# Performance work log

Measured on AMD Instinct MI355X. Metric: run time of the kernel, lower is better.

## Reference

```python
import jax, jax.numpy as jnp
import numpy as np

N_NODES = 50000
N_EDGES = 800000
IN_NODE = 64
IN_EDGE = 32
HIDDEN = 128
NUM_LAYERS = 3
OUT_DIM = 8
NUM_GRAPHS = 128


def setup_inputs() -> dict:
    key = jax.random.key(0)
    ks = jax.random.split(key, 20)
    inp = {
        "x": jax.random.normal(ks[0], (N_NODES, IN_NODE), dtype=jnp.float32),
        "edge_index": jax.random.randint(ks[1], (2, N_EDGES), 0, N_NODES, dtype=jnp.int32),
        "edge_attr": jax.random.normal(ks[2], (N_EDGES, IN_EDGE), dtype=jnp.float32),
        "batch": jnp.sort(jax.random.randint(ks[3], (N_NODES,), 0, NUM_GRAPHS, dtype=jnp.int32)),
    }
    # MLP params per GINEConv layer: Linear(d_in, H) -> ReLU -> Linear(H, H)
    d_ins = [IN_NODE + IN_EDGE] + [HIDDEN + IN_EDGE] * (NUM_LAYERS - 1)
    for i, d_in in enumerate(d_ins):
        inp[f"w{i}_1"] = jax.random.normal(ks[4 + 3 * i], (d_in, HIDDEN), dtype=jnp.float32) * (1.0 / np.sqrt(d_in))
        inp[f"b{i}_1"] = jnp.zeros((HIDDEN,), dtype=jnp.float32)
        inp[f"w{i}_2"] = jax.random.normal(ks[5 + 3 * i], (HIDDEN, HIDDEN), dtype=jnp.float32) * (1.0 / np.sqrt(HIDDEN))
        inp[f"b{i}_2"] = jnp.zeros((HIDDEN,), dtype=jnp.float32)
    inp["lin_w"] = jax.random.normal(ks[15], (HIDDEN, OUT_DIM), dtype=jnp.float32) * (1.0 / np.sqrt(HIDDEN))
    inp["lin_b"] = jnp.zeros((OUT_DIM,), dtype=jnp.float32)
    return inp


def _gine_conv(x, src, dst, edge_attr, w1, b1, w2, b2):
    # gather source node feats, concat with edge feats, 2-layer MLP, scatter-add to dst
    m = jnp.concatenate([x[src], edge_attr], axis=-1)        # [E, d_in]
    h = jax.nn.relu(m @ w1 + b1) @ w2 + b2                   # [E, H]
    return jax.ops.segment_sum(h, dst, num_segments=N_NODES)  # [N, H]


def reference(x, edge_index, edge_attr, batch,
              w0_1, b0_1, w0_2, b0_2,
              w1_1, b1_1, w1_2, b1_2,
              w2_1, b2_1, w2_2, b2_2,
              lin_w, lin_b):
    src, dst = edge_index[0], edge_index[1]
    layers = [(w0_1, b0_1, w0_2, b0_2), (w1_1, b1_1, w1_2, b1_2), (w2_1, b2_1, w2_2, b2_2)]
    h = x
    for (w1, b1, w2, b2) in layers:
        h = jax.nn.relu(_gine_conv(h, src, dst, edge_attr, w1, b1, w2, b2))
    # global mean pool over graphs
    sums = jax.ops.segment_sum(h, batch, num_segments=NUM_GRAPHS)          # [G, H]
    cnts = jax.ops.segment_sum(jnp.ones((N_NODES,), h.dtype), batch, num_segments=NUM_GRAPHS)
    pooled = sums / jnp.maximum(cnts, 1.0)[:, None]
    return pooled @ lin_w + lin_b
```

## Files before the change

kernel.cpp:

```cpp
#include <hip/hip_runtime.h>
#include <hip/hip_bf16.h>
#include <stdint.h>

typedef __attribute__((ext_vector_type(8))) __bf16 bf16x8;
typedef __attribute__((ext_vector_type(4))) __bf16 bf16x4;
typedef __attribute__((ext_vector_type(4))) float f32x4;

static constexpr int NN = 50000;
static constexpr int NE = 800000;
static constexpr int FX = 64;
static constexpr int FE = 32;
static constexpr int H  = 128;
static constexpr int NG = 128;
static constexpr int OD = 8;

__global__ void cvt_f32_bf16(const float* __restrict__ in, __bf16* __restrict__ out, int n) {
  int idx = (blockIdx.x * blockDim.x + threadIdx.x) * 4;
  if (idx + 3 < n) {
    float4 v = *reinterpret_cast<const float4*>(in + idx);
    bf16x4 o;
    o[0] = (__bf16)v.x; o[1] = (__bf16)v.y; o[2] = (__bf16)v.z; o[3] = (__bf16)v.w;
    *reinterpret_cast<bf16x4*>(out + idx) = o;
  } else {
    for (; idx < n; ++idx) out[idx] = (__bf16)in[idx];
  }
}

__global__ void cvt_w_t(const float* __restrict__ w, __bf16* __restrict__ wt, int K) {
  int i = blockIdx.x * blockDim.x + threadIdx.x;
  if (i >= K * 128) return;
  int n = i / K, k = i % K;
  wt[i] = (__bf16)w[k * 128 + n];
}

__global__ void hist_build(const int* __restrict__ dst, int* __restrict__ hist) {
  int e = blockIdx.x * blockDim.x + threadIdx.x;
  if (e < NE) atomicAdd(&hist[dst[e]], 1);
}

__global__ void scan1(const int* __restrict__ hist, int* __restrict__ excl, int* __restrict__ btot) {
  __shared__ int tmp[256];
  int t = threadIdx.x;
  int i = blockIdx.x * 256 + t;
  int v = (i < NN) ? hist[i] : 0;
  tmp[t] = v;
  __syncthreads();
  for (int off = 1; off < 256; off <<= 1) {
    int add = (t >= off) ? tmp[t - off] : 0;
    __syncthreads();
    tmp[t] += add;
    __syncthreads();
  }
  if (i < NN) excl[i] = tmp[t] - v;
  if (t == 255) btot[blockIdx.x] = tmp[255];
}

__global__ void scan2(int* __restrict__ btot, int nb) {
  __shared__ int tmp[256];
  int t = threadIdx.x;
  int v = (t < nb) ? btot[t] : 0;
  tmp[t] = v;
  __syncthreads();
  for (int off = 1; off < 256; off <<= 1) {
    int add = (t >= off) ? tmp[t - off] : 0;
    __syncthreads();
    tmp[t] += add;
    __syncthreads();
  }
  if (t < nb) btot[t] = tmp[t] - v;
}

__global__ void scan3(const int* __restrict__ excl, const int* __restrict__ btot,
                      int* __restrict__ cursor) {
  int i = blockIdx.x * 256 + threadIdx.x;
  if (i < NN) cursor[i] = excl[i] + btot[blockIdx.x];
}

__global__ void scatter_perm(const int* __restrict__ src, const int* __restrict__ dst,
                             int* __restrict__ cursor,
                             int* __restrict__ srcp, int* __restrict__ dstp,
                             int* __restrict__ eperm) {
  int e = blockIdx.x * blockDim.x + threadIdx.x;
  if (e >= NE) return;
  int d = dst[e];
  int p = atomicAdd(&cursor[d], 1);
  srcp[p] = src[e];
  dstp[p] = d;
  eperm[p] = e;
}

__global__ void sort_ea(const float* __restrict__ ea, const int* __restrict__ eperm,
                        __bf16* __restrict__ eabs) {
  int i = blockIdx.x * blockDim.x + threadIdx.x;
  if (i >= NE * 4) return;
  int p = i >> 2, c = i & 3;
  int e = eperm[p];
  float4 v0 = *reinterpret_cast<const float4*>(ea + (size_t)e * FE + c * 8);
  float4 v1 = *reinterpret_cast<const float4*>(ea + (size_t)e * FE + c * 8 + 4);
  bf16x8 o;
  o[0] = (__bf16)v0.x; o[1] = (__bf16)v0.y; o[2] = (__bf16)v0.z; o[3] = (__bf16)v0.w;
  o[4] = (__bf16)v1.x; o[5] = (__bf16)v1.y; o[6] = (__bf16)v1.z; o[7] = (__bf16)v1.w;
  *reinterpret_cast<bf16x8*>(eabs + (size_t)p * FE + c * 8) = o;
}

template<int F, int DIN>
__global__ __launch_bounds__(512) void node_gemm2(
    const __bf16* __restrict__ Ain,
    const __bf16* __restrict__ wt,
    __bf16* __restrict__ Y)
{
  constexpr int APAD = F + 8;
  constexpr int KS   = F / 32;
  constexpr int CH   = F / 8;
  constexpr int AB   = 128 * APAD * 2;
  constexpr int OB   = 128 * 136 * 2;
  constexpr int SB   = (AB > OB) ? AB : OB;
  __shared__ __align__(16) char smem[SB];
  auto As  = reinterpret_cast<__bf16 (*)[APAD]>(smem);
  auto Ost = reinterpret_cast<__bf16 (*)[136]>(smem);

  const int tid   = threadIdx.x;
  const int lane  = tid & 63;
  const int w     = tid >> 6;
  const int m0    = blockIdx.x * 128;
  const int colq  = lane & 15;
  const int krow  = (lane >> 4) * 8;
  const int rbase = (lane >> 4) * 4;
  const int col   = w * 16 + colq;

  bf16x8 bf[KS];
#pragma unroll
  for (int ks = 0; ks < KS; ++ks)
    bf[ks] = *reinterpret_cast<const bf16x8*>(wt + (size_t)col * DIN + ks * 32 + krow);

  for (int i = tid; i < 128 * CH; i += 512) {
    int row = i / CH, c = i % CH;
    int g = m0 + row; if (g >= NN) g = NN - 1;
    *reinterpret_cast<bf16x8*>(&As[row][c * 8]) =
        *reinterpret_cast<const bf16x8*>(Ain + (size_t)g * F + c * 8);
  }
  __syncthreads();

  f32x4 acc[8];
#pragma unroll
  for (int mt = 0; mt < 8; ++mt) acc[mt] = (f32x4){0.f, 0.f, 0.f, 0.f};
#pragma unroll
  for (int ks = 0; ks < KS; ++ks)
#pragma unroll
    for (int mt = 0; mt < 8; ++mt) {
      bf16x8 a = *reinterpret_cast<const bf16x8*>(&As[mt * 16 + colq][ks * 32 + krow]);
      acc[mt] = __builtin_amdgcn_mfma_f32_16x16x32_bf16(a, bf[ks], acc[mt], 0, 0, 0);
    }
  __syncthreads();

#pragma unroll
  for (int mt = 0; mt < 8; ++mt)
#pragma unroll
    for (int r = 0; r < 4; ++r)
      Ost[mt * 16 + rbase + r][col] = (__bf16)acc[mt][r];
  __syncthreads();

  for (int i = tid; i < 128 * 16; i += 512) {
    int row = i >> 4, c = i & 15;
    int g = m0 + row;
    if (g < NN)
      *reinterpret_cast<bf16x8*>(Y + (size_t)g * H + c * 8) =
          *reinterpret_cast<const bf16x8*>(&Ost[row][c * 8]);
  }
}

template<bool WRITE_Y>
__global__ __launch_bounds__(512) void node_wy(
    const float* __restrict__ aggHin,
    const int* __restrict__ deg,
    const __bf16* __restrict__ w2t,
    const float* __restrict__ b2,
    const __bf16* __restrict__ w1t,
    __bf16* __restrict__ Y,
    float* __restrict__ hpre)
{
  __shared__ __bf16 Ast[128][136];
  __shared__ __bf16 Hst[WRITE_Y ? 128 : 1][136];
  __shared__ int deg_s[128];

  const int tid   = threadIdx.x;
  const int lane  = tid & 63;
  const int w     = tid >> 6;
  const int m0    = blockIdx.x * 128;
  const int colq  = lane & 15;
  const int krow  = (lane >> 4) * 8;
  const int rbase = (lane >> 4) * 4;
  const int col   = w * 16 + colq;

  for (int i = tid; i < 128 * 16; i += 512) {
    int row = i >> 4, cb = (i & 15) * 8;
    int g = m0 + row; if (g >= NN) g = NN - 1;
    const float* s = aggHin + (size_t)g * H + cb;
    float4 v0 = *reinterpret_cast<const float4*>(s);
    float4 v1 = *reinterpret_cast<const float4*>(s + 4);
    bf16x8 o;
    o[0] = (__bf16)v0.x; o[1] = (__bf16)v0.y; o[2] = (__bf16)v0.z; o[3] = (__bf16)v0.w;
    o[4] = (__bf16)v1.x; o[5] = (__bf16)v1.y; o[6] = (__bf16)v1.z; o[7] = (__bf16)v1.w;
    *reinterpret_cast<bf16x8*>(&Ast[row][cb]) = o;
  }
  if (tid < 128) {
    int g = m0 + tid;
    deg_s[tid] = (g < NN) ? deg[g] : 0;
  }
  __syncthreads();

  bf16x8 w2f[4];
#pragma unroll
  for (int ks = 0; ks < 4; ++ks)
    w2f[ks] = *reinterpret_cast<const bf16x8*>(w2t + (size_t)col * H + ks * 32 + krow);
  const float b2s = b2[col];

  f32x4 acc[8];
#pragma unroll
  for (int mt = 0; mt < 8; ++mt) acc[mt] = (f32x4){0.f, 0.f, 0.f, 0.f};
#pragma unroll
  for (int ks = 0; ks < 4; ++ks)
#pragma unroll
    for (int mt = 0; mt < 8; ++mt) {
      bf16x8 a = *reinterpret_cast<const bf16x8*>(&Ast[mt * 16 + colq][ks * 32 + krow]);
      acc[mt] = __builtin_amdgcn_mfma_f32_16x16x32_bf16(a, w2f[ks], acc[mt], 0, 0, 0);
    }

  if (WRITE_Y) {
#pragma unroll
    for (int mt = 0; mt < 8; ++mt)
#pragma unroll
      for (int r = 0; r < 4; ++r) {
        int row = mt * 16 + rbase + r;
        float v = acc[mt][r] + (float)deg_s[row] * b2s;
        Hst[row][col] = (__bf16)fmaxf(v, 0.f);
      }
    __syncthreads();

    bf16x8 w1f[4];
#pragma unroll
    for (int ks = 0; ks < 4; ++ks)
      w1f[ks] = *reinterpret_cast<const bf16x8*>(w1t + (size_t)col * 160 + ks * 32 + krow);

    f32x4 acc2[8];
#pragma unroll
    for (int mt = 0; mt < 8; ++mt) acc2[mt] = (f32x4){0.f, 0.f, 0.f, 0.f};
#pragma unroll
    for (int ks = 0; ks < 4; ++ks)
#pragma unroll
      for (int mt = 0; mt < 8; ++mt) {
        bf16x8 a = *reinterpret_cast<const bf16x8*>(&Hst[mt * 16 + colq][ks * 32 + krow]);
        acc2[mt] = __builtin_amdgcn_mfma_f32_16x16x32_bf16(a, w1f[ks], acc2[mt], 0, 0, 0);
      }

#pragma unroll
    for (int mt = 0; mt < 8; ++mt)
#pragma unroll
      for (int r = 0; r < 4; ++r)
        Ast[mt * 16 + rbase + r][col] = (__bf16)acc2[mt][r];
    __syncthreads();

    for (int i = tid; i < 128 * 16; i += 512) {
      int row = i >> 4, cb = (i & 15) * 8;
      int g = m0 + row;
      if (g < NN)
        *reinterpret_cast<bf16x8*>(Y + (size_t)g * H + cb) =
            *reinterpret_cast<const bf16x8*>(&Ast[row][cb]);
    }
  } else {
#pragma unroll
    for (int mt = 0; mt < 8; ++mt)
#pragma unroll
      for (int r = 0; r < 4; ++r) {
        int row = mt * 16 + rbase + r;
        int g = m0 + row;
        if (g < NN)
          hpre[(size_t)g * H + col] = acc[mt][r] + (float)deg_s[row] * b2s;
      }
  }
}

template<int DIN>
__global__ __launch_bounds__(512) void edge_mlp4(
    const __bf16* __restrict__ Yb,
    const __bf16* __restrict__ eabs,
    const int* __restrict__ srcp, const int* __restrict__ dstp,
    const __bf16* __restrict__ w1t,
    const float* __restrict__ b1,
    float* __restrict__ aggH,
    int ntiles)
{
  constexpr int F = DIN - 32;
  constexpr int TPB = 4;
  __shared__ __bf16 Ylds[128][128];
  __shared__ int dst_s[128];

  const int tid   = threadIdx.x;
  const int lane  = tid & 63;
  const int w     = tid >> 6;
  const int colq  = lane & 15;
  const int krow  = (lane >> 4) * 8;
  const int rbase = (lane >> 4) * 4;
  const int col   = w * 16 + colq;

  const bf16x8 b1f = *reinterpret_cast<const bf16x8*>(w1t + (size_t)col * DIN + F + krow);
  const float  b1s = b1[col];

  const int yrow = tid >> 4;
  const int yc   = tid & 15;
  const int drow = tid & 127;

  int t0 = blockIdx.x * TPB;
  int t1 = t0 + TPB; if (t1 > ntiles) t1 = ntiles;
  if (t0 >= ntiles) return;

  int e0 = t0 * 128;
  int sA[4];
#pragma unroll
  for (int k = 0; k < 4; ++k) sA[k] = srcp[e0 + yrow + 32 * k];
  int dreg = dstp[e0 + drow];
  bf16x8 yreg[4];
#pragma unroll
  for (int k = 0; k < 4; ++k)
    yreg[k] = *reinterpret_cast<const bf16x8*>(Yb + (size_t)sA[k] * H + yc * 8);
  bf16x8 aef[8];
#pragma unroll
  for (int mt = 0; mt < 8; ++mt)
    aef[mt] = *reinterpret_cast<const bf16x8*>(eabs + (size_t)(e0 + mt * 16 + colq) * FE + krow);
  {
    int e0n = (t0 + 1 < t1) ? (t0 + 1) * 128 : e0;
#pragma unroll
    for (int k = 0; k < 4; ++k) sA[k] = srcp[e0n + yrow + 32 * k];
  }

  for (int t = t0; t < t1; ++t) {
    __syncthreads();
#pragma unroll
    for (int k = 0; k < 4; ++k) {
      int row = yrow + 32 * k;
      int cb = (yc * 8 + ((row >> 2) & 3) * 16) & 127;
      *reinterpret_cast<bf16x8*>(&Ylds[row][cb]) = yreg[k];
    }
    if (tid < 128) dst_s[tid] = dreg;
    __syncthreads();

    if (t + 1 < t1) {
      int e1 = (t + 1) * 128;
#pragma unroll
      for (int k = 0; k < 4; ++k)
        yreg[k] = *reinterpret_cast<const bf16x8*>(Yb + (size_t)sA[k] * H + yc * 8);
      dreg = dstp[e1 + drow];
      int e2 = (t + 2 < t1) ? (t + 2) * 128 : e1;
#pragma unroll
      for (int k = 0; k < 4; ++k) sA[k] = srcp[e2 + yrow + 32 * k];
    }

    f32x4 acc[8];
#pragma unroll
    for (int mt = 0; mt < 8; ++mt) acc[mt] = (f32x4){b1s, b1s, b1s, b1s};
#pragma unroll
    for (int mt = 0; mt < 8; ++mt)
      acc[mt] = __builtin_amdgcn_mfma_f32_16x16x32_bf16(aef[mt], b1f, acc[mt], 0, 0, 0);

    if (t + 1 < t1) {
      int e1 = (t + 1) * 128;
#pragma unroll
      for (int mt = 0; mt < 8; ++mt)
        aef[mt] = *reinterpret_cast<const bf16x8*>(eabs + (size_t)(e1 + mt * 16 + colq) * FE + krow);
    }

#pragma unroll
    for (int mt = 0; mt < 8; ++mt)
#pragma unroll
      for (int r = 0; r < 4; ++r) {
        int row = mt * 16 + rbase + r;
        int cs = (col + ((row >> 2) & 3) * 16) & 127;
        float v = (float)Ylds[row][cs] + acc[mt][r];
        Ylds[row][cs] = (__bf16)fmaxf(v, 0.f);
      }
    __syncthreads();

    {
      const int rc = tid & 127;
      const int r0 = (tid >> 7) * 32;
      float s = 0.f;
      int d = dst_s[r0];
#pragma unroll 4
      for (int r = r0; r < r0 + 32; ++r) {
        int dn = dst_s[r];
        float v = (float)Ylds[r][(rc + ((r >> 2) & 3) * 16) & 127];
        if (dn != d) { atomicAdd(aggH + (size_t)d * H + rc, s); s = 0.f; d = dn; }
        s += v;
      }
      atomicAdd(aggH + (size_t)d * H + rc, s);
    }
  }
}

__global__ void pool_kernel(const float* __restrict__ agg, const int* __restrict__ batch,
                            float* __restrict__ sums, float* __restrict__ cnts) {
  const int col = threadIdx.x & 127;
  const int sub = threadIdx.x >> 7;
  const int NB = 128;
  int n0 = blockIdx.x * NB + sub * (NB / 2);
  if (n0 >= NN) return;
  int n1 = n0 + NB / 2; if (n1 > NN) n1 = NN;
  float s = 0.f, c = 0.f;
  int g = batch[n0];
  for (int n = n0; n < n1; ++n) {
    int gn = batch[n];
    if (gn != g) {
      atomicAdd(&sums[g * H + col], s);
      if (col == 0) atomicAdd(&cnts[g], c);
      s = 0.f; c = 0.f; g = gn;
    }
    s += fmaxf(agg[(size_t)n * H + col], 0.f);
    c += 1.f;
  }
  atomicAdd(&sums[g * H + col], s);
  if (col == 0) atomicAdd(&cnts[g], c);
}

__global__ void final_kernel(const float* __restrict__ sums, const float* __restrict__ cnts,
                             const float* __restrict__ lw, const float* __restrict__ lb,
                             float* __restrict__ out) {
  int idx = blockIdx.x * blockDim.x + threadIdx.x;
  if (idx >= NG * OD) return;
  int g = idx / OD, o = idx % OD;
  float inv = 1.f / fmaxf(cnts[g], 1.f);
  float s = 0.f;
#pragma unroll 8
  for (int k = 0; k < H; ++k)
    s += sums[g * H + k] * lw[k * OD + o];
  out[idx] = s * inv + lb[o];
}

extern "C" void kernel_launch(void* const* d_in, const int* in_sizes, int n_in,
                              void* d_out, int out_size, void* d_ws, size_t ws_size,
                              hipStream_t stream) {
  const float* x   = (const float*)d_in[0];
  const int*   ei  = (const int*)d_in[1];
  const float* ea  = (const float*)d_in[2];
  const int*   bat = (const int*)d_in[3];
  const float* w1[3] = {(const float*)d_in[4], (const float*)d_in[8],  (const float*)d_in[12]};
  const float* b1[3] = {(const float*)d_in[5], (const float*)d_in[9],  (const float*)d_in[13]};
  const float* w2[3] = {(const float*)d_in[6], (const float*)d_in[10], (const float*)d_in[14]};
  const float* b2[3] = {(const float*)d_in[7], (const float*)d_in[11], (const float*)d_in[15]};
  const float* lw  = (const float*)d_in[16];
  const float* lb  = (const float*)d_in[17];
  float* out = (float*)d_out;

  char* ws = (char*)d_ws;
  size_t off = 0;
  auto alloc = [&](size_t bytes) -> void* {
    void* p = ws + off;
    off = (off + bytes + 255) & ~(size_t)255;
    return p;
  };
  __bf16* xb   = (__bf16*)alloc((size_t)NN * FX * 2);
  __bf16* Yb   = (__bf16*)alloc((size_t)NN * H * 2);
  __bf16* eabs = (__bf16*)alloc((size_t)NE * FE * 2);
  float*  agg  = (float*) alloc((size_t)NN * H * 4);
  __bf16* w1t[3]; __bf16* w2t[3];
  for (int l = 0; l < 3; ++l) {
    w1t[l] = (__bf16*)alloc(128 * 160 * 2);
    w2t[l] = (__bf16*)alloc(128 * 128 * 2);
  }
  float* sums = (float*)alloc(NG * H * 4);
  float* cnts = (float*)alloc(NG * 4);
  int* hist   = (int*)alloc((size_t)NN * 4);
  int* excl   = (int*)alloc((size_t)NN * 4);
  int* btot   = (int*)alloc(256 * 4);
  int* cursor = (int*)alloc((size_t)NN * 4);
  int* srcp   = (int*)alloc((size_t)NE * 4);
  int* dstp   = (int*)alloc((size_t)NE * 4);
  int* eperm  = (int*)alloc((size_t)NE * 4);

  const int* src = ei;
  const int* dst = ei + NE;
  const int NB_SCAN = (NN + 255) / 256;
  const int NTILES = NE / 128;
  const int EGRID  = (NTILES + 3) / 4;
  const int NGRID  = (NN + 127) / 128;

  cvt_f32_bf16<<<(NN * FX / 4 + 255) / 256, 256, 0, stream>>>(x, xb, NN * FX);
  const int dins[3] = {96, 160, 160};
  for (int l = 0; l < 3; ++l) {
    cvt_w_t<<<(dins[l] * 128 + 255) / 256, 256, 0, stream>>>(w1[l], w1t[l], dins[l]);
    cvt_w_t<<<(128 * 128 + 255) / 256, 256, 0, stream>>>(w2[l], w2t[l], 128);
  }

  hipMemsetAsync(hist, 0, (size_t)NN * 4, stream);
  hist_build<<<(NE + 255) / 256, 256, 0, stream>>>(dst, hist);
  scan1<<<NB_SCAN, 256, 0, stream>>>(hist, excl, btot);
  scan2<<<1, 256, 0, stream>>>(btot, NB_SCAN);
  scan3<<<NB_SCAN, 256, 0, stream>>>(excl, btot, cursor);
  scatter_perm<<<(NE + 255) / 256, 256, 0, stream>>>(src, dst, cursor, srcp, dstp, eperm);
  sort_ea<<<(NE * 4 + 255) / 256, 256, 0, stream>>>(ea, eperm, eabs);

  node_gemm2<64, 96><<<NGRID, 512, 0, stream>>>(xb, w1t[0], Yb);
  hipMemsetAsync(agg, 0, (size_t)NN * H * 4, stream);
  edge_mlp4<96><<<EGRID, 512, 0, stream>>>(Yb, eabs, srcp, dstp, w1t[0], b1[0], agg, NTILES);

  for (int l = 1; l < 3; ++l) {
    node_wy<true><<<NGRID, 512, 0, stream>>>(agg, hist, w2t[l - 1], b2[l - 1],
                                             w1t[l], Yb, nullptr);
    hipMemsetAsync(agg, 0, (size_t)NN * H * 4, stream);
    edge_mlp4<160><<<EGRID, 512, 0, stream>>>(Yb, eabs, srcp, dstp, w1t[l], b1[l], agg, NTILES);
  }

  node_wy<false><<<NGRID, 512, 0, stream>>>(agg, hist, w2t[2], b2[2],
                                            nullptr, nullptr, agg);
  hipMemsetAsync(sums, 0, NG * H * 4, stream);
  hipMemsetAsync(cnts, 0, NG * 4, stream);
  pool_kernel<<<(NN + 127) / 128, 256, 0, stream>>>(agg, bat, sums, cnts);
  final_kernel<<<(NG * OD + 255) / 256, 256, 0, stream>>>(sums, cnts, lw, lb, out);
}
```

Before: 481.4 us.

## Fuse weight conversions, edge-attr sort, agg zeroing, and final pooling into fewer kernels

Merges the six weight-transpose launches into one kernel and folds the edge-attribute permutation into the scatter kernel, which drops the eperm buffer. The node kernel now zeroes agg as it reads it, so the per-layer memsets go away. The last node GEMM pools directly into the per-graph sums with run-length atomics, removing the fp32 hpre write and the separate pool kernel. Graph counts now come from a small integer histogram. The intent is fewer launches and less global traffic, at the cost of uncoalesced per-thread edge-attr reads in the scatter and more atomics in the pooling step.

New measurement: 533.9 us. 10.9% more time.

```diff
diff --git a/kernel.cpp b/kernel.cpp
--- a/kernel.cpp
+++ b/kernel.cpp
@@ -26,11 +26,24 @@
   }
 }
 
-__global__ void cvt_w_t(const float* __restrict__ w, __bf16* __restrict__ wt, int K) {
+__global__ void cvt_w_all(const float* __restrict__ a0, const float* __restrict__ a1,
+                          const float* __restrict__ a2, const float* __restrict__ a3,
+                          const float* __restrict__ a4, const float* __restrict__ a5,
+                          __bf16* __restrict__ o0, __bf16* __restrict__ o1,
+                          __bf16* __restrict__ o2, __bf16* __restrict__ o3,
+                          __bf16* __restrict__ o4, __bf16* __restrict__ o5) {
   int i = blockIdx.x * blockDim.x + threadIdx.x;
-  if (i >= K * 128) return;
-  int n = i / K, k = i % K;
-  wt[i] = (__bf16)w[k * 128 + n];
+  const float* src; __bf16* dst; int K; int base;
+  if      (i <  12288) { src = a0; dst = o0; K =  96; base = 0; }
+  else if (i <  32768) { src = a1; dst = o1; K = 160; base = 12288; }
+  else if (i <  53248) { src = a2; dst = o2; K = 160; base = 32768; }
+  else if (i <  69632) { src = a3; dst = o3; K = 128; base = 53248; }
+  else if (i <  86016) { src = a4; dst = o4; K = 128; base = 69632; }
+  else if (i < 102400) { src = a5; dst = o5; K = 128; base = 86016; }
+  else return;
+  int j = i - base;
+  int n = j / K, k = j % K;
+  dst[j] = (__bf16)src[k * 128 + n];
 }
 
 __global__ void hist_build(const int* __restrict__ dst, int* __restrict__ hist) {
@@ -76,31 +89,28 @@
   if (i < NN) cursor[i] = excl[i] + btot[blockIdx.x];
 }
 
-__global__ void scatter_perm(const int* __restrict__ src, const int* __restrict__ dst,
-                             int* __restrict__ cursor,
-                             int* __restrict__ srcp, int* __restrict__ dstp,
-                             int* __restrict__ eperm) {
+__global__ void scatter_perm_ea(const int* __restrict__ src, const int* __restrict__ dst,
+                                const float* __restrict__ ea,
+                                int* __restrict__ cursor,
+                                int* __restrict__ srcp, int* __restrict__ dstp,
+                                __bf16* __restrict__ eabs) {
   int e = blockIdx.x * blockDim.x + threadIdx.x;
   if (e >= NE) return;
   int d = dst[e];
   int p = atomicAdd(&cursor[d], 1);
   srcp[p] = src[e];
   dstp[p] = d;
-  eperm[p] = e;
-}
-
-__global__ void sort_ea(const float* __restrict__ ea, const int* __restrict__ eperm,
-                        __bf16* __restrict__ eabs) {
-  int i = blockIdx.x * blockDim.x + threadIdx.x;
-  if (i >= NE * 4) return;
-  int p = i >> 2, c = i & 3;
-  int e = eperm[p];
-  float4 v0 = *reinterpret_cast<const float4*>(ea + (size_t)e * FE + c * 8);
-  float4 v1 = *reinterpret_cast<const float4*>(ea + (size_t)e * FE + c * 8 + 4);
-  bf16x8 o;
-  o[0] = (__bf16)v0.x; o[1] = (__bf16)v0.y; o[2] = (__bf16)v0.z; o[3] = (__bf16)v0.w;
-  o[4] = (__bf16)v1.x; o[5] = (__bf16)v1.y; o[6] = (__bf16)v1.z; o[7] = (__bf16)v1.w;
-  *reinterpret_cast<bf16x8*>(eabs + (size_t)p * FE + c * 8) = o;
+  const float* er = ea + (size_t)e * FE;
+  __bf16* op = eabs + (size_t)p * FE;
+#pragma unroll
+  for (int c = 0; c < 4; ++c) {
+    float4 v0 = *reinterpret_cast<const float4*>(er + c * 8);
+    float4 v1 = *reinterpret_cast<const float4*>(er + c * 8 + 4);
+    bf16x8 o;
+    o[0] = (__bf16)v0.x; o[1] = (__bf16)v0.y; o[2] = (__bf16)v0.z; o[3] = (__bf16)v0.w;
+    o[4] = (__bf16)v1.x; o[5] = (__bf16)v1.y; o[6] = (__bf16)v1.z; o[7] = (__bf16)v1.w;
+    *reinterpret_cast<bf16x8*>(op + c * 8) = o;
+  }
 }
 
 template<int F, int DIN>
@@ -169,18 +179,16 @@
   }
 }
 
-template<bool WRITE_Y>
-__global__ __launch_bounds__(512) void node_wy(
-    const float* __restrict__ aggHin,
+__global__ __launch_bounds__(512) void node_wy_t(
+    float* __restrict__ aggH,
     const int* __restrict__ deg,
     const __bf16* __restrict__ w2t,
     const float* __restrict__ b2,
     const __bf16* __restrict__ w1t,
-    __bf16* __restrict__ Y,
-    float* __restrict__ hpre)
+    __bf16* __restrict__ Y)
 {
   __shared__ __bf16 Ast[128][136];
-  __shared__ __bf16 Hst[WRITE_Y ? 128 : 1][136];
+  __shared__ __bf16 Hst[128][136];
   __shared__ int deg_s[128];
 
   const int tid   = threadIdx.x;
@@ -194,14 +202,20 @@
 
   for (int i = tid; i < 128 * 16; i += 512) {
     int row = i >> 4, cb = (i & 15) * 8;
-    int g = m0 + row; if (g >= NN) g = NN - 1;
-    const float* s = aggHin + (size_t)g * H + cb;
+    int g = m0 + row;
+    bool valid = g < NN;
+    int gc = valid ? g : NN - 1;
+    float* s = aggH + (size_t)gc * H + cb;
     float4 v0 = *reinterpret_cast<const float4*>(s);
     float4 v1 = *reinterpret_cast<const float4*>(s + 4);
     bf16x8 o;
     o[0] = (__bf16)v0.x; o[1] = (__bf16)v0.y; o[2] = (__bf16)v0.z; o[3] = (__bf16)v0.w;
     o[4] = (__bf16)v1.x; o[5] = (__bf16)v1.y; o[6] = (__bf16)v1.z; o[7] = (__bf16)v1.w;
     *reinterpret_cast<bf16x8*>(&Ast[row][cb]) = o;
+    if (valid) {
+      *reinterpret_cast<float4*>(s)     = (float4){0.f, 0.f, 0.f, 0.f};
+      *reinterpret_cast<float4*>(s + 4) = (float4){0.f, 0.f, 0.f, 0.f};
+    }
   }
   if (tid < 128) {
     int g = m0 + tid;
@@ -226,58 +240,121 @@
       acc[mt] = __builtin_amdgcn_mfma_f32_16x16x32_bf16(a, w2f[ks], acc[mt], 0, 0, 0);
     }
 
-  if (WRITE_Y) {
-#pragma unroll
-    for (int mt = 0; mt < 8; ++mt)
-#pragma unroll
-      for (int r = 0; r < 4; ++r) {
-        int row = mt * 16 + rbase + r;
-        float v = acc[mt][r] + (float)deg_s[row] * b2s;
-        Hst[row][col] = (__bf16)fmaxf(v, 0.f);
+#pragma unroll
+  for (int mt = 0; mt < 8; ++mt)
+#pragma unroll
+    for (int r = 0; r < 4; ++r) {
+      int row = mt * 16 + rbase + r;
+      float v = acc[mt][r] + (float)deg_s[row] * b2s;
+      Hst[row][col] = (__bf16)fmaxf(v, 0.f);
+    }
+  __syncthreads();
+
+  bf16x8 w1f[4];
+#pragma unroll
+  for (int ks = 0; ks < 4; ++ks)
+    w1f[ks] = *reinterpret_cast<const bf16x8*>(w1t + (size_t)col * 160 + ks * 32 + krow);
+
+  f32x4 acc2[8];
+#pragma unroll
+  for (int mt = 0; mt < 8; ++mt) acc2[mt] = (f32x4){0.f, 0.f, 0.f, 0.f};
+#pragma unroll
+  for (int ks = 0; ks < 4; ++ks)
+#pragma unroll
+    for (int mt = 0; mt < 8; ++mt) {
+      bf16x8 a = *reinterpret_cast<const bf16x8*>(&Hst[mt * 16 + colq][ks * 32 + krow]);
+      acc2[mt] = __builtin_amdgcn_mfma_f32_16x16x32_bf16(a, w1f[ks], acc2[mt], 0, 0, 0);
+    }
+
+#pragma unroll
+  for (int mt = 0; mt < 8; ++mt)
+#pragma unroll
+    for (int r = 0; r < 4; ++r)
+      Ast[mt * 16 + rbase + r][col] = (__bf16)acc2[mt][r];
+  __syncthreads();
+
+  for (int i = tid; i < 128 * 16; i += 512) {
+    int row = i >> 4, cb = (i & 15) * 8;
+    int g = m0 + row;
+    if (g < NN)
+      *reinterpret_cast<bf16x8*>(Y + (size_t)g * H + cb) =
+          *reinterpret_cast<const bf16x8*>(&Ast[row][cb]);
+  }
+}
+
+__global__ __launch_bounds__(512) void node_pool(
+    const float* __restrict__ aggH,
+    const int* __restrict__ deg,
+    const __bf16* __restrict__ w2t,
+    const float* __restrict__ b2,
+    const int* __restrict__ batch,
+    float* __restrict__ sums)
+{
+  __shared__ __bf16 Ast[128][136];
+  __shared__ int deg_s[128];
+  __shared__ int bs[128];
+
+  const int tid   = threadIdx.x;
+  const int lane  = tid & 63;
+  const int w     = tid >> 6;
+  const int m0    = blockIdx.x * 128;
+  const int colq  = lane & 15;
+  const int krow  = (lane >> 4) * 8;
+  const int rbase = (lane >> 4) * 4;
+  const int col   = w * 16 + colq;
+
+  for (int i = tid; i < 128 * 16; i += 512) {
+    int row = i >> 4, cb = (i & 15) * 8;
+    int g = m0 + row; if (g >= NN) g = NN - 1;
+    const float* s = aggH + (size_t)g * H + cb;
+    float4 v0 = *reinterpret_cast<const float4*>(s);
+    float4 v1 = *reinterpret_cast<const float4*>(s + 4);
+    bf16x8 o;
+    o[0] = (__bf16)v0.x; o[1] = (__bf16)v0.y; o[2] = (__bf16)v0.z; o[3] = (__bf16)v0.w;
+    o[4] = (__bf16)v1.x; o[5] = (__bf16)v1.y; o[6] = (__bf16)v1.z; o[7] = (__bf16)v1.w;
+    *reinterpret_cast<bf16x8*>(&Ast[row][cb]) = o;
+  }
+  if (tid < 128) {
+    int g = m0 + tid;
+    deg_s[tid] = (g < NN) ? deg[g] : 0;
+    bs[tid]    = (g < NN) ? batch[g] : -1;
+  }
+  __syncthreads();
+
+  bf16x8 w2f[4];
+#pragma unroll
+  for (int ks = 0; ks < 4; ++ks)
+    w2f[ks] = *reinterpret_cast<const bf16x8*>(w2t + (size_t)col * H + ks * 32 + krow);
+  const float b2s = b2[col];
+
+  f32x4 acc[8];
+#pragma unroll
+  for (int mt = 0; mt < 8; ++mt) acc[mt] = (f32x4){0.f, 0.f, 0.f, 0.f};
+#pragma unroll
+  for (int ks = 0; ks < 4; ++ks)
+#pragma unroll
+    for (int mt = 0; mt < 8; ++mt) {
+      bf16x8 a = *reinterpret_cast<const bf16x8*>(&Ast[mt * 16 + colq][ks * 32 + krow]);
+      acc[mt] = __builtin_amdgcn_mfma_f32_16x16x32_bf16(a, w2f[ks], acc[mt], 0, 0, 0);
+    }
+
+  float run = 0.f;
+  int cur = -2;
+#pragma unroll
+  for (int mt = 0; mt < 8; ++mt)
+#pragma unroll
+    for (int r = 0; r < 4; ++r) {
+      int row = mt * 16 + rbase + r;
+      int b = bs[row];
+      float v = fmaxf(acc[mt][r] + (float)deg_s[row] * b2s, 0.f);
+      if (b != cur) {
+        if (cur >= 0) atomicAdd(&sums[cur * H + col], run);
+        run = 0.f;
+        cur = b;
       }
-    __syncthreads();
-
-    bf16x8 w1f[4];
-#pragma unroll
-    for (int ks = 0; ks < 4; ++ks)
-      w1f[ks] = *reinterpret_cast<const bf16x8*>(w1t + (size_t)col * 160 + ks * 32 + krow);
-
-    f32x4 acc2[8];
-#pragma unroll
-    for (int mt = 0; mt < 8; ++mt) acc2[mt] = (f32x4){0.f, 0.f, 0.f, 0.f};
-#pragma unroll
-    for (int ks = 0; ks < 4; ++ks)
-#pragma unroll
-      for (int mt = 0; mt < 8; ++mt) {
-        bf16x8 a = *reinterpret_cast<const bf16x8*>(&Hst[mt * 16 + colq][ks * 32 + krow]);
-        acc2[mt] = __builtin_amdgcn_mfma_f32_16x16x32_bf16(a, w1f[ks], acc2[mt], 0, 0, 0);
-      }
-
-#pragma unroll
-    for (int mt = 0; mt < 8; ++mt)
-#pragma unroll
-      for (int r = 0; r < 4; ++r)
-        Ast[mt * 16 + rbase + r][col] = (__bf16)acc2[mt][r];
-    __syncthreads();
-
-    for (int i = tid; i < 128 * 16; i += 512) {
-      int row = i >> 4, cb = (i & 15) * 8;
-      int g = m0 + row;
-      if (g < NN)
-        *reinterpret_cast<bf16x8*>(Y + (size_t)g * H + cb) =
-            *reinterpret_cast<const bf16x8*>(&Ast[row][cb]);
-    }
-  } else {
-#pragma unroll
-    for (int mt = 0; mt < 8; ++mt)
-#pragma unroll
-      for (int r = 0; r < 4; ++r) {
-        int row = mt * 16 + rbase + r;
-        int g = m0 + row;
-        if (g < NN)
-          hpre[(size_t)g * H + col] = acc[mt][r] + (float)deg_s[row] * b2s;
-      }
-  }
+      if (b >= 0) run += v;
+    }
+  if (cur >= 0) atomicAdd(&sums[cur * H + col], run);
 }
 
 template<int DIN>
@@ -397,37 +474,19 @@
   }
 }
 
-__global__ void pool_kernel(const float* __restrict__ agg, const int* __restrict__ batch,
-                            float* __restrict__ sums, float* __restrict__ cnts) {
-  const int col = threadIdx.x & 127;
-  const int sub = threadIdx.x >> 7;
-  const int NB = 128;
-  int n0 = blockIdx.x * NB + sub * (NB / 2);
-  if (n0 >= NN) return;
-  int n1 = n0 + NB / 2; if (n1 > NN) n1 = NN;
-  float s = 0.f, c = 0.f;
-  int g = batch[n0];
-  for (int n = n0; n < n1; ++n) {
-    int gn = batch[n];
-    if (gn != g) {
-      atomicAdd(&sums[g * H + col], s);
-      if (col == 0) atomicAdd(&cnts[g], c);
-      s = 0.f; c = 0.f; g = gn;
-    }
-    s += fmaxf(agg[(size_t)n * H + col], 0.f);
-    c += 1.f;
-  }
-  atomicAdd(&sums[g * H + col], s);
-  if (col == 0) atomicAdd(&cnts[g], c);
-}
-
-__global__ void final_kernel(const float* __restrict__ sums, const float* __restrict__ cnts,
+__global__ void cnt_hist(const int* __restrict__ batch, int* __restrict__ cnti) {
+  int n = blockIdx.x * blockDim.x + threadIdx.x;
+  if (n < NN) atomicAdd(&cnti[batch[n]], 1);
+}
+
+__global__ void final_kernel(const float* __restrict__ sums, const int* __restrict__ cnti,
                              const float* __restrict__ lw, const float* __restrict__ lb,
                              float* __restrict__ out) {
   int idx = blockIdx.x * blockDim.x + threadIdx.x;
   if (idx >= NG * OD) return;
   int g = idx / OD, o = idx % OD;
-  float inv = 1.f / fmaxf(cnts[g], 1.f);
+  float c = (float)cnti[g];
+  float inv = 1.f / fmaxf(c, 1.f);
   float s = 0.f;
 #pragma unroll 8
   for (int k = 0; k < H; ++k)
@@ -467,14 +526,13 @@
     w2t[l] = (__bf16*)alloc(128 * 128 * 2);
   }
   float* sums = (float*)alloc(NG * H * 4);
-  float* cnts = (float*)alloc(NG * 4);
+  int*   cnti = (int*)  alloc(NG * 4);
   int* hist   = (int*)alloc((size_t)NN * 4);
   int* excl   = (int*)alloc((size_t)NN * 4);
   int* btot   = (int*)alloc(256 * 4);
   int* cursor = (int*)alloc((size_t)NN * 4);
   int* srcp   = (int*)alloc((size_t)NE * 4);
   int* dstp   = (int*)alloc((size_t)NE * 4);
-  int* eperm  = (int*)alloc((size_t)NE * 4);
 
   const int* src = ei;
   const int* dst = ei + NE;
@@ -483,36 +541,30 @@
   const int EGRID  = (NTILES + 3) / 4;
   const int NGRID  = (NN + 127) / 128;
 
+  hipMemsetAsync(agg, 0, (size_t)NN * H * 4, stream);
+  hipMemsetAsync(sums, 0, (size_t)NG * H * 4 + 256 + NG * 4, stream);
+
   cvt_f32_bf16<<<(NN * FX / 4 + 255) / 256, 256, 0, stream>>>(x, xb, NN * FX);
-  const int dins[3] = {96, 160, 160};
-  for (int l = 0; l < 3; ++l) {
-    cvt_w_t<<<(dins[l] * 128 + 255) / 256, 256, 0, stream>>>(w1[l], w1t[l], dins[l]);
-    cvt_w_t<<<(128 * 128 + 255) / 256, 256, 0, stream>>>(w2[l], w2t[l], 128);
-  }
+  cvt_w_all<<<(102400 + 255) / 256, 256, 0, stream>>>(
+      w1[0], w1[1], w1[2], w2[0], w2[1], w2[2],
+      w1t[0], w1t[1], w1t[2], w2t[0], w2t[1], w2t[2]);
 
   hipMemsetAsync(hist, 0, (size_t)NN * 4, stream);
   hist_build<<<(NE + 255) / 256, 256, 0, stream>>>(dst, hist);
   scan1<<<NB_SCAN, 256, 0, stream>>>(hist, excl, btot);
   scan2<<<1, 256, 0, stream>>>(btot, NB_SCAN);
   scan3<<<NB_SCAN, 256, 0, stream>>>(excl, btot, cursor);
-  scatter_perm<<<(NE + 255) / 256, 256, 0, stream>>>(src, dst, cursor, srcp, dstp, eperm);
-  sort_ea<<<(NE * 4 + 255) / 256, 256, 0, stream>>>(ea, eperm, eabs);
+  scatter_perm_ea<<<(NE + 255) / 256, 256, 0, stream>>>(src, dst, ea, cursor, srcp, dstp, eabs);
 
   node_gemm2<64, 96><<<NGRID, 512, 0, stream>>>(xb, w1t[0], Yb);
-  hipMemsetAsync(agg, 0, (size_t)NN * H * 4, stream);
   edge_mlp4<96><<<EGRID, 512, 0, stream>>>(Yb, eabs, srcp, dstp, w1t[0], b1[0], agg, NTILES);
 
   for (int l = 1; l < 3; ++l) {
-    node_wy<true><<<NGRID, 512, 0, stream>>>(agg, hist, w2t[l - 1], b2[l - 1],
-                                             w1t[l], Yb, nullptr);
-    hipMemsetAsync(agg, 0, (size_t)NN * H * 4, stream);
+    node_wy_t<<<NGRID, 512, 0, stream>>>(agg, hist, w2t[l - 1], b2[l - 1], w1t[l], Yb);
     edge_mlp4<160><<<EGRID, 512, 0, stream>>>(Yb, eabs, srcp, dstp, w1t[l], b1[l], agg, NTILES);
   }
 
-  node_wy<false><<<NGRID, 512, 0, stream>>>(agg, hist, w2t[2], b2[2],
-                                            nullptr, nullptr, agg);
-  hipMemsetAsync(sums, 0, NG * H * 4, stream);
-  hipMemsetAsync(cnts, 0, NG * 4, stream);
-  pool_kernel<<<(NN + 127) / 128, 256, 0, stream>>>(agg, bat, sums, cnts);
-  final_kernel<<<(NG * OD + 255) / 256, 256, 0, stream>>>(sums, cnts, lw, lb, out);
-}
+  node_pool<<<NGRID, 512, 0, stream>>>(agg, hist, w2t[2], b2[2], bat, sums);
+  cnt_hist<<<(NN + 255) / 256, 256, 0, stream>>>(bat, cnti);
+  final_kernel<<<(NG * OD + 255) / 256, 256, 0, stream>>>(sums, cnti, lw, lb, out);
+}
```
